# Kernel tuning notes

Hardware: AMD Instinct MI355X
Metric: run time of the kernel (lower is better)

The kernel has to match this reference:

```python
import jax, jax.numpy as jnp
import numpy as np

N_NODES = 50000
N_EDGES = 800000
D_FEAT = 128
EMBED_DIM = 128
NUM_HEADS = 8
HEAD_DIM = EMBED_DIM // NUM_HEADS


def mish(x):
    return x * jnp.tanh(jax.nn.softplus(x))


def setup_inputs() -> dict:
    key = jax.random.key(0)
    ks = jax.random.split(key, 8)
    nodes = jax.random.normal(ks[0], (N_NODES, D_FEAT), dtype=jnp.float32)
    senders = jax.random.randint(ks[1], (N_EDGES,), 0, N_NODES, dtype=jnp.int32)
    receivers = jax.random.randint(ks[2], (N_EDGES,), 0, N_NODES, dtype=jnp.int32)
    s = 1.0 / np.sqrt(D_FEAT)
    Ws_k = jax.random.normal(ks[3], (D_FEAT, NUM_HEADS, HEAD_DIM), dtype=jnp.float32) * s
    Ws_b = jnp.zeros((NUM_HEADS, HEAD_DIM), dtype=jnp.float32)
    Wr_k = jax.random.normal(ks[4], (D_FEAT, NUM_HEADS, HEAD_DIM), dtype=jnp.float32) * s
    Wr_b = jnp.zeros((NUM_HEADS, HEAD_DIM), dtype=jnp.float32)
    attn_k = jax.random.normal(ks[5], (HEAD_DIM, 1), dtype=jnp.float32) / np.sqrt(HEAD_DIM)
    attn_b = jnp.zeros((1,), dtype=jnp.float32)
    return {"nodes": nodes, "senders": senders, "receivers": receivers,
            "Ws_k": Ws_k, "Ws_b": Ws_b, "Wr_k": Wr_k, "Wr_b": Wr_b,
            "attn_k": attn_k, "attn_b": attn_b}


def reference(nodes, senders, receivers, Ws_k, Ws_b, Wr_k, Wr_b, attn_k, attn_b):
    # gather endpoint features along edges
    sent = nodes[senders]        # [E, F]
    recv = nodes[receivers]      # [E, F]
    # edge messages: W_s(sent) -> [E, H, D]
    edges = jnp.einsum('ef,fhd->ehd', sent, Ws_k) + Ws_b
    # attention logits: Dense(1)(mish(edges + W_r(recv))) -> [E, H, 1]
    x = mish(edges + jnp.einsum('ef,fhd->ehd', recv, Wr_k) + Wr_b)
    logits = jnp.einsum('ehd,do->eho', x, attn_k) + attn_b  # [E, H, 1]
    # segment softmax over incoming edges of each receiver node
    seg_max = jax.ops.segment_max(logits, receivers, num_segments=N_NODES)  # [N, H, 1]
    unnorm = jnp.exp(logits - seg_max[receivers])
    denom = jax.ops.segment_sum(unnorm, receivers, num_segments=N_NODES)   # [N, H, 1]
    weights = unnorm / denom[receivers]                                     # [E, H, 1]
    # attention-weighted scatter-add into receiver nodes
    agg = jax.ops.segment_sum(edges * weights, receivers, num_segments=N_NODES)  # [N, H, D]
    # node update: concat heads
    return agg.reshape(N_NODES, NUM_HEADS * HEAD_DIM)
```

## Files before the change

### kernel.cpp

```cpp
#include <hip/hip_runtime.h>

#define N_NODES 50000
#define N_EDGES 800000
#define HEADS 8
#define HD 16
#define F 128
#define RPB 16
#define SCAN_B 1024
#define NB1 ((N_NODES + SCAN_B - 1) / SCAN_B)
#define TILE 8

__device__ __forceinline__ float head16_sum(float x) {
    int v;
    v = __builtin_amdgcn_update_dpp(0, __float_as_int(x), 0xB1, 0xF, 0xF, true);
    x += __int_as_float(v);
    v = __builtin_amdgcn_update_dpp(0, __float_as_int(x), 0x4E, 0xF, 0xF, true);
    x += __int_as_float(v);
    v = __builtin_amdgcn_update_dpp(0, __float_as_int(x), 0x141, 0xF, 0xF, true);
    x += __int_as_float(v);
    v = __builtin_amdgcn_update_dpp(0, __float_as_int(x), 0x140, 0xF, 0xF, true);
    x += __int_as_float(v);
    return x;
}

__global__ __launch_bounds__(128) void k_proj_hist(
        const float* __restrict__ nodes,
        const float* __restrict__ Ws, const float* __restrict__ Wsb,
        const float* __restrict__ Wr, const float* __restrict__ Wrb,
        const int* __restrict__ receivers, int* __restrict__ counts,
        float* __restrict__ Ps, float* __restrict__ Pr) {
    __shared__ float rows[RPB][F];
    const int o  = threadIdx.x;
    const int r0 = blockIdx.x * RPB;

    const int ebase = blockIdx.x * 256 + o;
    atomicAdd(counts + receivers[ebase], 1);
    atomicAdd(counts + receivers[ebase + 128], 1);

    for (int i = 0; i < RPB; ++i)
        rows[i][o] = nodes[(r0 + i) * F + o];
    __syncthreads();

    float accs[RPB], accr[RPB];
    const float bs = Wsb[o], br = Wrb[o];
    #pragma unroll
    for (int i = 0; i < RPB; ++i) { accs[i] = bs; accr[i] = br; }

    for (int f = 0; f < F; ++f) {
        const float ws = Ws[f * F + o];
        const float wr = Wr[f * F + o];
        #pragma unroll
        for (int i = 0; i < RPB; ++i) {
            accs[i] = fmaf(rows[i][f], ws, accs[i]);
            accr[i] = fmaf(rows[i][f], wr, accr[i]);
        }
    }
    #pragma unroll
    for (int i = 0; i < RPB; ++i) {
        Ps[(r0 + i) * F + o] = accs[i];
        Pr[(r0 + i) * F + o] = accr[i];
    }
}

__global__ __launch_bounds__(1024) void k_scan1(
        const int* __restrict__ counts, int* __restrict__ starts,
        int* __restrict__ partials) {
    __shared__ int buf[SCAN_B];
    const int i = blockIdx.x * SCAN_B + threadIdx.x;
    const int v = (i < N_NODES) ? counts[i] : 0;
    buf[threadIdx.x] = v;
    __syncthreads();
    for (int off = 1; off < SCAN_B; off <<= 1) {
        const int t = (threadIdx.x >= (unsigned)off) ? buf[threadIdx.x - off] : 0;
        __syncthreads();
        buf[threadIdx.x] += t;
        __syncthreads();
    }
    if (i < N_NODES) starts[i] = buf[threadIdx.x] - v;
    if (threadIdx.x == SCAN_B - 1) partials[blockIdx.x] = buf[SCAN_B - 1];
}

__global__ __launch_bounds__(256) void k_fill(
        const int* __restrict__ senders, const int* __restrict__ receivers,
        const int* __restrict__ starts, const int* __restrict__ partials,
        int* __restrict__ cursor, int* __restrict__ slist) {
    __shared__ int off_lds[NB1];
    if (threadIdx.x < 64) {
        const int j = (int)threadIdx.x;
        const int v = (j < NB1) ? partials[j] : 0;
        int incl = v;
        #pragma unroll
        for (int d = 1; d < 64; d <<= 1) {
            const int u = __shfl_up(incl, d);
            if (j >= d) incl += u;
        }
        if (j < NB1) off_lds[j] = incl - v;
    }
    __syncthreads();
    const int e = blockIdx.x * 256 + (int)threadIdx.x;
    const int r = receivers[e];
    const int pos = atomicAdd(cursor + r, 1);
    slist[starts[r] + off_lds[r >> 10] + pos] = senders[e];
}

__global__ __launch_bounds__(128) void k_agg_fused(
        const int* __restrict__ starts, const int* __restrict__ counts,
        const int* __restrict__ partials, const int* __restrict__ slist,
        const float* __restrict__ Ps, const float* __restrict__ Pr,
        const float* __restrict__ attn_k,
        float* __restrict__ out) {
    const int n = blockIdx.x;
    const int t = threadIdx.x;

    const int sb = n >> 10;
    const int lane = t & 63;
    int v = (lane < sb) ? partials[lane] : 0;
    v += __shfl_xor(v, 1);  v += __shfl_xor(v, 2);  v += __shfl_xor(v, 4);
    v += __shfl_xor(v, 8);  v += __shfl_xor(v, 16); v += __shfl_xor(v, 32);

    const int e0 = starts[n] + v;
    const int e1 = e0 + counts[n];
    const float pr = Pr[n * F + t];
    const float ak = attn_k[t & 15];

    float den = 0.0f, acc = 0.0f;

    for (int i = e0; i < e1; i += TILE) {
        float psv[TILE];
        #pragma unroll
        for (int k = 0; k < TILE; ++k) {
            const int idx = (i + k < e1) ? (i + k) : (e1 - 1);
            psv[k] = Ps[slist[idx] * F + t];
        }
        #pragma unroll
        for (int k = 0; k < TILE; ++k) {
            const float x  = psv[k] + pr;
            const float ex = __expf(x);
            const float z  = 1.0f + ex;
            const float zz = fmaf(z, z, 1.0f);
            const float r  = __builtin_amdgcn_rcpf(zz);
            const float mi = fmaf(-2.0f * x, r, x) * ak;
            const float sum = head16_sum(mi);
            const float w = (i + k < e1) ? __expf(sum) : 0.0f;
            den += w;
            acc = fmaf(w, psv[k], acc);
        }
    }
    out[n * F + t] = (den > 0.0f) ? acc / den : 0.0f;
}

extern "C" void kernel_launch(void* const* d_in, const int* in_sizes, int n_in,
                              void* d_out, int out_size, void* d_ws, size_t ws_size,
                              hipStream_t stream) {
    const float* nodes     = (const float*)d_in[0];
    const int*   senders   = (const int*)  d_in[1];
    const int*   receivers = (const int*)  d_in[2];
    const float* Wsk       = (const float*)d_in[3];
    const float* Wsb       = (const float*)d_in[4];
    const float* Wrk       = (const float*)d_in[5];
    const float* Wrb       = (const float*)d_in[6];
    const float* attnk     = (const float*)d_in[7];
    float* out = (float*)d_out;

    float* Ps       = (float*)d_ws;
    float* Pr       = Ps + (size_t)N_NODES * F;
    int*   slist    = (int*)(Pr + (size_t)N_NODES * F);
    int*   counts   = slist + N_EDGES;
    int*   cursor   = counts + N_NODES;
    int*   starts   = cursor + N_NODES;
    int*   partials = starts + N_NODES + 1;

    hipMemsetAsync(counts, 0, 2 * N_NODES * sizeof(int), stream);

    k_proj_hist<<<N_NODES / RPB, 128, 0, stream>>>(nodes, Wsk, Wsb, Wrk, Wrb,
                                                   receivers, counts, Ps, Pr);
    k_scan1<<<NB1, SCAN_B, 0, stream>>>(counts, starts, partials);
    k_fill<<<N_EDGES / 256, 256, 0, stream>>>(senders, receivers, starts,
                                              partials, cursor, slist);
    k_agg_fused<<<N_NODES, 128, 0, stream>>>(starts, counts, partials, slist,
                                             Ps, Pr, attnk, out);
}
```

Before: 312.2 us.

## Map one wavefront per node with float2 lanes and prefetch next edge tile

The aggregation kernel now gives each receiver node a single 64-lane wavefront, four nodes per 256-thread block, instead of a 128-thread block. Each lane handles two feature dims through float2 loads, so the per-head reduction drops to three DPP steps over 8 lanes. The next tile of sender rows is loaded into registers while the current tile is computed. This aims to cut block count and scheduling overhead, halve the shuffle work per edge, and hide gather latency, at the cost of more registers per thread and two mish evaluations per lane.

```diff
diff --git a/kernel.cpp b/kernel.cpp
--- a/kernel.cpp
+++ b/kernel.cpp
@@ -10,15 +10,21 @@
 #define NB1 ((N_NODES + SCAN_B - 1) / SCAN_B)
 #define TILE 8
 
-__device__ __forceinline__ float head16_sum(float x) {
+__device__ __forceinline__ float mish_x(float x) {
+    const float ex = __expf(x);
+    const float z  = 1.0f + ex;
+    const float zz = fmaf(z, z, 1.0f);
+    const float r  = __builtin_amdgcn_rcpf(zz);
+    return fmaf(-2.0f * x, r, x);
+}
+
+__device__ __forceinline__ float head8_sum(float x) {
     int v;
     v = __builtin_amdgcn_update_dpp(0, __float_as_int(x), 0xB1, 0xF, 0xF, true);
     x += __int_as_float(v);
     v = __builtin_amdgcn_update_dpp(0, __float_as_int(x), 0x4E, 0xF, 0xF, true);
     x += __int_as_float(v);
     v = __builtin_amdgcn_update_dpp(0, __float_as_int(x), 0x141, 0xF, 0xF, true);
-    x += __int_as_float(v);
-    v = __builtin_amdgcn_update_dpp(0, __float_as_int(x), 0x140, 0xF, 0xF, true);
     x += __int_as_float(v);
     return x;
 }
@@ -103,50 +109,65 @@
     slist[starts[r] + off_lds[r >> 10] + pos] = senders[e];
 }
 
-__global__ __launch_bounds__(128) void k_agg_fused(
+__global__ __launch_bounds__(256) void k_agg_fused(
         const int* __restrict__ starts, const int* __restrict__ counts,
         const int* __restrict__ partials, const int* __restrict__ slist,
         const float* __restrict__ Ps, const float* __restrict__ Pr,
-        const float* __restrict__ attn_k,
-        float* __restrict__ out) {
-    const int n = blockIdx.x;
-    const int t = threadIdx.x;
+        const float* __restrict__ attn_k, float* __restrict__ out) {
+    const int lane = (int)threadIdx.x & 63;
+    const int n = __builtin_amdgcn_readfirstlane(
+                      blockIdx.x * 4 + ((int)threadIdx.x >> 6));
+    const int d0 = lane << 1;
 
     const int sb = n >> 10;
-    const int lane = t & 63;
     int v = (lane < sb) ? partials[lane] : 0;
     v += __shfl_xor(v, 1);  v += __shfl_xor(v, 2);  v += __shfl_xor(v, 4);
     v += __shfl_xor(v, 8);  v += __shfl_xor(v, 16); v += __shfl_xor(v, 32);
 
     const int e0 = starts[n] + v;
     const int e1 = e0 + counts[n];
-    const float pr = Pr[n * F + t];
-    const float ak = attn_k[t & 15];
-
-    float den = 0.0f, acc = 0.0f;
-
-    for (int i = e0; i < e1; i += TILE) {
-        float psv[TILE];
+    const float2 pr2 = *(const float2*)(Pr + (size_t)n * F + d0);
+    const float2 ak2 = *(const float2*)(attn_k + (d0 & 15));
+
+    float den = 0.0f, ax = 0.0f, ay = 0.0f;
+
+    if (e1 > e0) {
+        float2 cur[TILE], nxt[TILE];
         #pragma unroll
         for (int k = 0; k < TILE; ++k) {
-            const int idx = (i + k < e1) ? (i + k) : (e1 - 1);
-            psv[k] = Ps[slist[idx] * F + t];
-        }
-        #pragma unroll
-        for (int k = 0; k < TILE; ++k) {
-            const float x  = psv[k] + pr;
-            const float ex = __expf(x);
-            const float z  = 1.0f + ex;
-            const float zz = fmaf(z, z, 1.0f);
-            const float r  = __builtin_amdgcn_rcpf(zz);
-            const float mi = fmaf(-2.0f * x, r, x) * ak;
-            const float sum = head16_sum(mi);
-            const float w = (i + k < e1) ? __expf(sum) : 0.0f;
-            den += w;
-            acc = fmaf(w, psv[k], acc);
-        }
-    }
-    out[n * F + t] = (den > 0.0f) ? acc / den : 0.0f;
+            const int idx = (e0 + k < e1) ? e0 + k : e1 - 1;
+            cur[k] = *(const float2*)(Ps + (size_t)slist[idx] * F + d0);
+        }
+        for (int i = e0; i < e1; i += TILE) {
+            const bool more = (i + TILE) < e1;
+            if (more) {
+                #pragma unroll
+                for (int k = 0; k < TILE; ++k) {
+                    const int idx = (i + TILE + k < e1) ? i + TILE + k : e1 - 1;
+                    nxt[k] = *(const float2*)(Ps + (size_t)slist[idx] * F + d0);
+                }
+            }
+            #pragma unroll
+            for (int k = 0; k < TILE; ++k) {
+                const float mi = mish_x(cur[k].x + pr2.x) * ak2.x
+                               + mish_x(cur[k].y + pr2.y) * ak2.y;
+                const float s = head8_sum(mi);
+                const float w = (i + k < e1) ? __expf(s) : 0.0f;
+                den += w;
+                ax = fmaf(w, cur[k].x, ax);
+                ay = fmaf(w, cur[k].y, ay);
+            }
+            if (more) {
+                #pragma unroll
+                for (int k = 0; k < TILE; ++k) cur[k] = nxt[k];
+            }
+        }
+    }
+    const float inv = __builtin_amdgcn_rcpf(den);
+    float2 o2;
+    o2.x = (den > 0.0f) ? ax * inv : 0.0f;
+    o2.y = (den > 0.0f) ? ay * inv : 0.0f;
+    *(float2*)(out + (size_t)n * F + d0) = o2;
 }
 
 extern "C" void kernel_launch(void* const* d_in, const int* in_sizes, int n_in,
@@ -177,6 +198,6 @@
     k_scan1<<<NB1, SCAN_B, 0, stream>>>(counts, starts, partials);
     k_fill<<<N_EDGES / 256, 256, 0, stream>>>(senders, receivers, starts,
                                               partials, cursor, slist);
-    k_agg_fused<<<N_NODES, 128, 0, stream>>>(starts, counts, partials, slist,
-                                             Ps, Pr, attnk, out);
-}
+    k_agg_fused<<<N_NODES / 4, 256, 0, stream>>>(starts, counts, partials,
+                                                 slist, Ps, Pr, attnk, out);
+}
```

Result: faster. 282.7 us (-9.4%).
